# Performance work log

Measured on AMD Instinct MI355X. Metric: run time of the kernel, lower is better.

The kernel has to match this reference:

```python
import jax, jax.numpy as jnp
import numpy as np

EPS_Q = 1e-4     # ridge added to L L^T in OptNet.forward
MAX_ITER = 20    # qpth pdipm_b maxIter
BIG = 1e10       # sentinel for inactive step-length entries


def _make_kkt_solver(Q, G):
    """Shared factorizations (qpth pre_factor_kkt): Q Cholesky and S0 = G Q^{-1} G^T."""
    nineq = G.shape[0]
    Lq = jnp.linalg.cholesky(Q)                                   # [nz, nz]

    def q_solve(rhs):                                             # rhs [B, nz] -> Q^{-1} rhs
        return jax.scipy.linalg.cho_solve((Lq, True), rhs.T).T

    S0 = G @ jax.scipy.linalg.cho_solve((Lq, True), G.T)          # [nineq, nineq]
    eye = jnp.eye(nineq, dtype=Q.dtype)

    def solve(d, rx, rs, rz):
        # Solve the reduced KKT system (qpth solve_kkt, neq=0):
        #   [Q G^T; G -D^{-1}] [dx; dz] = [-rx; -rz + D^{-1} rs],  ds = (-rs - dz)/d
        invQ_rx = q_solve(rx)                                     # [B, nz]
        hv = invQ_rx @ G.T + rs / d - rz                          # [B, nineq]
        S = S0[None] + eye * (1.0 / d)[:, None, :]                # S0 + diag(1/d) per batch
        dz = -jnp.linalg.solve(S, hv[..., None])[..., 0]
        dx = q_solve(-rx - dz @ G)
        ds = (-rs - dz) / d
        return dx, ds, dz

    return solve


def _get_step(v, dv):
    # max alpha with v + alpha*dv >= 0 (min over entries with dv < 0); safe against NaN grads
    dv_safe = jnp.where(dv < 0, dv, -1.0)
    a = jnp.where(dv < 0, -v / dv_safe, BIG)
    return jnp.min(a, axis=1)


def pdipm_forward(Q, p, G, h):
    """qpth pdipm_b.forward (Mehrotra predictor-corrector), neq=0, fixed 20 iters with best-tracking."""
    nB, nz = p.shape
    nineq = G.shape[0]
    solve = _make_kkt_solver(Q, G)

    # initial point: KKT solve with d = 1, then shift s, z into the positive orthant
    d0 = jnp.ones((nB, nineq), Q.dtype)
    zeros = jnp.zeros((nB, nineq), Q.dtype)
    x, s, z = solve(d0, p, zeros, -h)
    smin = jnp.min(s, axis=1, keepdims=True)
    s = jnp.where(smin < 0, s - smin + 1.0, s)
    zmin = jnp.min(z, axis=1, keepdims=True)
    z = jnp.where(zmin < 0, z - zmin + 1.0, z)

    def body(carry, _):
        x, s, z, bx, bz, bs, bsum = carry
        rx = x @ Q + p + z @ G          # stationarity residual (Q symmetric)
        rs = z
        rz = x @ G.T + s - h            # primal residual
        mu = jnp.abs(jnp.sum(s * z, axis=1)) / nineq
        resids = jnp.linalg.norm(rz, axis=1) + jnp.linalg.norm(rx, axis=1) + nineq * mu
        rsum = jnp.sum(resids)
        imp = rsum < bsum
        bx = jnp.where(imp, x, bx)
        bz = jnp.where(imp, z, bz)
        bs = jnp.where(imp, s, bs)
        bsum = jnp.where(imp, rsum, bsum)
        d = z / s
        # affine (predictor) step
        dx_a, ds_a, dz_a = solve(d, rx, rs, rz)
        alpha = jnp.minimum(jnp.minimum(_get_step(z, dz_a), _get_step(s, ds_a)), 1.0)[:, None]
        sig = (jnp.sum((s + alpha * ds_a) * (z + alpha * dz_a), axis=1)
               / jnp.sum(s * z, axis=1)) ** 3
        # centering + corrector step
        rs_c = ((-mu * sig)[:, None] + ds_a * dz_a) / s
        dx_c, ds_c, dz_c = solve(d, jnp.zeros_like(rx), rs_c, jnp.zeros_like(rz))
        dx = dx_a + dx_c
        ds = ds_a + ds_c
        dz = dz_a + dz_c
        alpha = jnp.minimum(0.999 * jnp.minimum(_get_step(z, dz), _get_step(s, ds)), 1.0)[:, None]
        x = x + alpha * dx
        s = s + alpha * ds
        z = z + alpha * dz
        return (x, s, z, bx, bz, bs, bsum), None

    init = (x, s, z, x, z, s, jnp.asarray(np.inf, dtype=Q.dtype))
    (x, s, z, bx, bz, bs, bsum), _ = jax.lax.scan(body, init, None, length=MAX_ITER)
    return bx, bz, bs                   # zhat, lam (dual), slack


def setup_inputs() -> dict:
    key = jax.random.key(0)
    k1, k2, k3 = jax.random.split(key, 3)
    B, nz, nineq = 128, 512, 512
    x = jax.random.normal(k1, (B, nz), dtype=jnp.float32)
    M = jnp.tril(jnp.ones((nz, nz), jnp.float32))                        # Parameter M = tril(ones)
    L = jnp.tril(jax.random.uniform(k2, (nz, nz), dtype=jnp.float32))    # Parameter L = tril(rand)
    G = jax.random.uniform(k3, (nineq, nz), dtype=jnp.float32, minval=-1.0, maxval=1.0)
    s0 = jnp.ones((nineq,), jnp.float32)
    z0 = jnp.zeros((nz,), jnp.float32)
    return {"x": x, "M": M, "L": L, "G": G, "s0": s0, "z0": z0}


def reference(x, M, L, G, s0, z0):
    nz = L.shape[0]
    Lm = M * L
    Q = Lm @ Lm.T + EPS_Q * jnp.eye(nz, dtype=L.dtype)                   # PSD + ridge
    h = jnp.broadcast_to(z0 @ G.T + s0, (x.shape[0], G.shape[0]))        # h = G z0 + s0
    zhat, _, _ = pdipm_forward(Q, x, G, h)                               # p = x
    return zhat
```

## Files before the change

kernel.cpp:

```cpp
#include <hip/hip_runtime.h>
#include <math.h>

#define BIGD 1e10
#define N2C 262144
#define PITCH_AS 257
#define FACF 131328

__device__ __forceinline__ int tile_off(int bi, int bj) {
    return 512 * bi * (bi - 1) + 528 * bi + (bj << 10);
}
__device__ __forceinline__ int tile_off_diag(int bi) {
    return 512 * bi * (bi - 1) + 528 * bi + (bi << 10);
}

__device__ __forceinline__ double blk_reduce_sum_d(double v, double* red) {
    int tid = threadIdx.x;
    red[tid] = v; __syncthreads();
    for (int s = 128; s > 0; s >>= 1) {
        if (tid < s) red[tid] += red[tid + s];
        __syncthreads();
    }
    double r = red[0]; __syncthreads();
    return r;
}
__device__ __forceinline__ double blk_reduce_min_d(double v, double* red) {
    int tid = threadIdx.x;
    red[tid] = v; __syncthreads();
    for (int s = 128; s > 0; s >>= 1) {
        if (tid < s) red[tid] = fmin(red[tid], red[tid + s]);
        __syncthreads();
    }
    double r = red[0]; __syncthreads();
    return r;
}

__global__ void k_lm(const float* __restrict__ M, const float* __restrict__ L,
                     double* __restrict__ C, int n) {
    int i = blockIdx.x * 256 + threadIdx.x;
    if (i < n) C[i] = (double)M[i] * (double)L[i];
}
__global__ void k_cast(const float* __restrict__ A, double* __restrict__ B, int n) {
    int i = blockIdx.x * 256 + threadIdx.x;
    if (i < n) B[i] = (double)A[i];
}
__global__ void k_cast32v(const double* __restrict__ A, float* __restrict__ B, int n) {
    int i = blockIdx.x * 256 + threadIdx.x;
    if (i < n) B[i] = (float)A[i];
}
__global__ void k_initbsum(double* bsum) {
    if (threadIdx.x == 0) bsum[0] = 1e300;
}

__global__ __launch_bounds__(256) void k_transpose_d(const double* __restrict__ A,
                                                     double* __restrict__ B) {
    __shared__ double t[32][33];
    int bx = blockIdx.x & 15, by = blockIdx.x >> 4;
    int x = threadIdx.x & 31, y0 = threadIdx.x >> 5;
#pragma unroll
    for (int l = 0; l < 4; ++l) {
        int y = y0 + 8 * l;
        t[y][x] = A[(size_t)(by * 32 + y) * 512 + bx * 32 + x];
    }
    __syncthreads();
#pragma unroll
    for (int l = 0; l < 4; ++l) {
        int y = y0 + 8 * l;
        B[(size_t)(bx * 32 + y) * 512 + by * 32 + x] = t[x][y];
    }
}
__global__ __launch_bounds__(256) void k_transpose32(const float* __restrict__ A,
                                                     float* __restrict__ B) {
    __shared__ float t[32][33];
    int bx = blockIdx.x & 15, by = blockIdx.x >> 4;
    int x = threadIdx.x & 31, y0 = threadIdx.x >> 5;
#pragma unroll
    for (int l = 0; l < 4; ++l) {
        int y = y0 + 8 * l;
        t[y][x] = A[(size_t)(by * 32 + y) * 512 + bx * 32 + x];
    }
    __syncthreads();
#pragma unroll
    for (int l = 0; l < 4; ++l) {
        int y = y0 + 8 * l;
        B[(size_t)(bx * 32 + y) * 512 + by * 32 + x] = t[x][y];
    }
}

__global__ void k_h_d(const float* __restrict__ G, const float* __restrict__ s0,
                      const float* __restrict__ z0, double* __restrict__ h) {
    __shared__ double red[256];
    int tid = threadIdx.x;
    int j = blockIdx.x * 64 + (tid >> 2);
    int q = tid & 3;
    double a = 0.0;
    for (int k = q * 128; k < q * 128 + 128; ++k)
        a += (double)G[(size_t)j * 512 + k] * (double)z0[k];
    red[tid] = a;
    __syncthreads();
    if (q == 0) h[j] = (double)s0[j] + red[tid] + red[tid + 1] + red[tid + 2] + red[tid + 3];
}

__global__ __launch_bounds__(256) void k_bgemm_d(
    const double* __restrict__ A1, const double* __restrict__ B1,
    double* __restrict__ C, double sgn, double diag_eps)
{
    __shared__ double As[32 * 68];
    __shared__ double Bs[32 * 68];
    int bid = blockIdx.x;
    int mt = bid >> 3, nt = bid & 7;
    int m0 = mt * 64, n0 = nt * 64;
    int tid = threadIdx.x;
    int tx = tid & 15, ty = tid >> 4;
    double acc[4][4] = {};
    for (int k0 = 0; k0 < 512; k0 += 32) {
        __syncthreads();
#pragma unroll
        for (int l = 0; l < 8; ++l) {
            int idx = tid + 256 * l;
            int kk = idx & 31, r = idx >> 5;
            As[kk * 68 + r] = A1[(size_t)(m0 + r) * 512 + k0 + kk];
            int cc = idx & 63, k2 = idx >> 6;
            Bs[k2 * 68 + cc] = B1[(size_t)(k0 + k2) * 512 + n0 + cc];
        }
        __syncthreads();
#pragma unroll
        for (int kk = 0; kk < 32; ++kk) {
            double a4[4], b4[4];
#pragma unroll
            for (int u = 0; u < 4; ++u) a4[u] = As[kk * 68 + tx * 4 + u];
#pragma unroll
            for (int u = 0; u < 4; ++u) b4[u] = Bs[kk * 68 + ty * 4 + u];
#pragma unroll
            for (int ii = 0; ii < 4; ++ii)
#pragma unroll
                for (int jj = 0; jj < 4; ++jj)
                    acc[ii][jj] += a4[ii] * b4[jj];
        }
    }
#pragma unroll
    for (int ii = 0; ii < 4; ++ii) {
        int gm = m0 + tx * 4 + ii;
#pragma unroll
        for (int jj = 0; jj < 4; ++jj) {
            int gn = n0 + ty * 4 + jj;
            double v = sgn * acc[ii][jj];
            if (diag_eps != 0.0 && gm == gn) v += diag_eps;
            C[(size_t)gm * 512 + gn] = v;
        }
    }
}

__global__ __launch_bounds__(256) void k_gemm32(
    const float* __restrict__ A1, const float* __restrict__ B1,
    const float* __restrict__ A2, const float* __restrict__ B2,
    float* __restrict__ C,
    const float* __restrict__ addp, const float* __restrict__ subp,
    const float* __restrict__ rowp, float rowsgn, float sgn)
{
    __shared__ float As[32 * 68];
    __shared__ float Bs[32 * 68];
    int bid = blockIdx.x;
    int mt = bid >> 3, nt = bid & 7;
    int m0 = mt * 64, n0 = nt * 64;
    int tid = threadIdx.x;
    int tx = tid & 15, ty = tid >> 4;
    double acc[4][4] = {};
    for (int prod = 0; prod < 2; ++prod) {
        const float* A = prod ? A2 : A1;
        const float* B = prod ? B2 : B1;
        if (A == nullptr) break;
        for (int k0 = 0; k0 < 512; k0 += 32) {
            __syncthreads();
#pragma unroll
            for (int l = 0; l < 8; ++l) {
                int idx = tid + 256 * l;
                int kk = idx & 31, r = idx >> 5;
                As[kk * 68 + r] = A[(size_t)(m0 + r) * 512 + k0 + kk];
                int cc = idx & 63, k2 = idx >> 6;
                Bs[k2 * 68 + cc] = B[(size_t)(k0 + k2) * 512 + n0 + cc];
            }
            __syncthreads();
#pragma unroll
            for (int kk = 0; kk < 32; ++kk) {
                double a4[4], b4[4];
#pragma unroll
                for (int u = 0; u < 4; ++u) a4[u] = (double)As[kk * 68 + tx * 4 + u];
#pragma unroll
                for (int u = 0; u < 4; ++u) b4[u] = (double)Bs[kk * 68 + ty * 4 + u];
#pragma unroll
                for (int ii = 0; ii < 4; ++ii)
#pragma unroll
                    for (int jj = 0; jj < 4; ++jj)
                        acc[ii][jj] += a4[ii] * b4[jj];
            }
        }
    }
#pragma unroll
    for (int ii = 0; ii < 4; ++ii) {
        int gm = m0 + tx * 4 + ii;
#pragma unroll
        for (int jj = 0; jj < 4; ++jj) {
            int gn = n0 + ty * 4 + jj;
            size_t gi = (size_t)gm * 512 + gn;
            double v = (double)sgn * acc[ii][jj];
            if (addp) v += (double)addp[gi];
            if (subp) v -= (double)subp[gi];
            if (rowp) v += (double)rowsgn * (double)rowp[gn];
            C[gi] = (float)v;
        }
    }
}

__global__ void k_copyadd_d(const double* __restrict__ S, double* __restrict__ F,
                            double dc, int n) {
    int i = blockIdx.x * 256 + threadIdx.x;
    if (i < n) {
        double v = S[i];
        if (dc != 0.0 && (i >> 9) == (i & 511)) v += dc;
        F[i] = v;
    }
}

__global__ __launch_bounds__(512) void k_cpanel_d(double* __restrict__ F, int kp) {
    int c0 = kp * 32, tid = threadIdx.x;
    __shared__ double Dl[32 * 33];
    __shared__ double rdg[32];
    if (tid < 32) {
        int i = tid;
        double d[32];
#pragma unroll
        for (int j = 0; j < 32; ++j) d[j] = F[(size_t)(c0 + i) * 512 + c0 + j];
#pragma unroll
        for (int j = 0; j < 32; ++j) {
            double djj = __shfl(d[j], j);
            djj = (djj > 1e-300) ? djj : 1e-300;
            double sj = sqrt(djj);
            double inv = 1.0 / sj;
            if (i == j) { d[j] = sj; rdg[j] = inv; }
            if (i > j) d[j] *= inv;
            double lij = d[j];
#pragma unroll
            for (int t = j + 1; t < 32; ++t) {
                double ltj = __shfl(d[j], t);
                if (i >= t) d[t] -= lij * ltj;
            }
        }
#pragma unroll
        for (int j = 0; j < 32; ++j) {
            if (j <= i) {
                Dl[i * 33 + j] = d[j];
                F[(size_t)(c0 + i) * 512 + c0 + j] = d[j];
            }
        }
    }
    __syncthreads();
    int r = c0 + 32 + tid;
    if (r < 512) {
        double p[32];
#pragma unroll
        for (int j = 0; j < 32; ++j) p[j] = F[(size_t)r * 512 + c0 + j];
#pragma unroll
        for (int j = 0; j < 32; ++j) {
            double pj = p[j] * rdg[j];
            p[j] = pj;
#pragma unroll
            for (int t = j + 1; t < 32; ++t) p[t] -= pj * Dl[t * 33 + j];
        }
#pragma unroll
        for (int j = 0; j < 32; ++j) F[(size_t)r * 512 + c0 + j] = p[j];
    }
}

__global__ __launch_bounds__(256) void k_syrk_d(double* __restrict__ F, int kp) {
    int c0 = kp * 32;
    int t = blockIdx.x;
    int bi = 0;
    while ((bi + 1) * (bi + 2) / 2 <= t) ++bi;
    int bj = t - bi * (bi + 1) / 2;
    int i0 = c0 + 32 + bi * 64, j0 = c0 + 32 + bj * 64;
    __shared__ double Pa[32 * 68], Pb[32 * 68];
    int tid = threadIdx.x;
#pragma unroll
    for (int l = 0; l < 8; ++l) {
        int idx = tid + 256 * l;
        int kk = idx & 31, r = idx >> 5;
        int ga = i0 + r, gb = j0 + r;
        Pa[kk * 68 + r] = (ga < 512) ? F[(size_t)ga * 512 + c0 + kk] : 0.0;
        Pb[kk * 68 + r] = (gb < 512) ? F[(size_t)gb * 512 + c0 + kk] : 0.0;
    }
    __syncthreads();
    int tx = tid & 15, ty = tid >> 4;
    double acc[4][4] = {};
#pragma unroll
    for (int kk = 0; kk < 32; ++kk) {
        double a4[4], b4[4];
#pragma unroll
        for (int u = 0; u < 4; ++u) a4[u] = Pa[kk * 68 + tx * 4 + u];
#pragma unroll
        for (int u = 0; u < 4; ++u) b4[u] = Pb[kk * 68 + ty * 4 + u];
#pragma unroll
        for (int ii = 0; ii < 4; ++ii)
#pragma unroll
            for (int jj = 0; jj < 4; ++jj)
                acc[ii][jj] += a4[ii] * b4[jj];
    }
#pragma unroll
    for (int ii = 0; ii < 4; ++ii) {
        int gi = i0 + tx * 4 + ii;
        if (gi < 512) {
#pragma unroll
            for (int jj = 0; jj < 4; ++jj) {
                int gj = j0 + ty * 4 + jj;
                if (gj < 512) F[(size_t)gi * 512 + gj] -= acc[ii][jj];
            }
        }
    }
}

__global__ __launch_bounds__(256) void k_solve_d(
    const double* __restrict__ F,
    const float* __restrict__ rhs32,
    double* __restrict__ o1, double* __restrict__ o2,
    float* __restrict__ o1f, float* __restrict__ o2f,
    int mode)
{
    int b = blockIdx.x;
    int tid = threadIdx.x;
    __shared__ double w[512];
    __shared__ double Ft[64 * 65];
    __shared__ double red[256];
    if (rhs32) {
        w[tid] = (double)rhs32[(size_t)b * 512 + tid];
        w[tid + 256] = (double)rhs32[(size_t)b * 512 + tid + 256];
    } else {
        w[tid] = (tid == b) ? 1.0 : 0.0;
        w[tid + 256] = (tid + 256 == b) ? 1.0 : 0.0;
    }
    for (int blk = 0; blk < 8; ++blk) {
        int c0 = blk * 64;
        int r = tid & 63, q = tid >> 6;
        double acc = 0.0;
        for (int jt = 0; jt < blk; ++jt) {
            __syncthreads();
#pragma unroll
            for (int l = 0; l < 16; ++l) {
                int idx = tid + 256 * l;
                int rr = idx >> 6, cc = idx & 63;
                Ft[rr * 65 + cc] = F[(size_t)(c0 + rr) * 512 + jt * 64 + cc];
            }
            __syncthreads();
#pragma unroll
            for (int jj = 0; jj < 16; ++jj) {
                int j = q * 16 + jj;
                acc += Ft[r * 65 + j] * w[jt * 64 + j];
            }
        }
        red[tid] = acc;
        __syncthreads();
#pragma unroll
        for (int l = 0; l < 16; ++l) {
            int idx = tid + 256 * l;
            int rr = idx >> 6, cc = idx & 63;
            Ft[rr * 65 + cc] = F[(size_t)(c0 + rr) * 512 + c0 + cc];
        }
        __syncthreads();
        if (tid < 64) {
            int i = tid;
            double a = w[c0 + i] - (red[i] + red[i + 64] + red[i + 128] + red[i + 192]);
            double rd = 1.0 / Ft[i * 65 + i];
#pragma unroll
            for (int j = 0; j < 64; ++j) {
                double wj = __shfl(a, j) * __shfl(rd, j);
                if (i == j) w[c0 + i] = wj;
                if (i > j) a -= Ft[i * 65 + j] * wj;
            }
        }
        __syncthreads();
    }
    for (int blk = 7; blk >= 0; --blk) {
        int c0 = blk * 64;
        __syncthreads();
#pragma unroll
        for (int l = 0; l < 16; ++l) {
            int idx = tid + 256 * l;
            int rr = idx >> 6, cc = idx & 63;
            Ft[rr * 65 + cc] = F[(size_t)(c0 + rr) * 512 + c0 + cc];
        }
        __syncthreads();
        if (tid < 64) {
            int i = tid;
            double a = w[c0 + i];
            double rd = 1.0 / Ft[i * 65 + i];
#pragma unroll
            for (int j = 63; j >= 0; --j) {
                double wj = __shfl(a, j) * __shfl(rd, j);
                if (i == j) w[c0 + i] = wj;
                if (i < j) a -= Ft[j * 65 + i] * wj;
            }
        }
        __syncthreads();
        if (c0 > 0) {
            for (int base = 0; base < c0; base += 256) {
                int col = base + tid;
                if (col < c0) {
                    double s = 0.0;
#pragma unroll
                    for (int i2 = 0; i2 < 64; ++i2)
                        s += F[(size_t)(c0 + i2) * 512 + col] * w[c0 + i2];
                    w[col] -= s;
                }
            }
        }
    }
    __syncthreads();
#pragma unroll
    for (int l = 0; l < 2; ++l) {
        int i = tid + l * 256;
        double wv = w[i];
        size_t gi = (size_t)b * 512 + i;
        if (mode == 0) {
            o1[gi] = wv;
            o1f[gi] = (float)wv;
        } else {
            o1[gi] = -wv;
            o2[gi] = wv;
            o1f[gi] = (float)(-wv);
            o2f[gi] = (float)wv;
        }
    }
}

__device__ void trsv_packed(const float* __restrict__ Lb, const double* __restrict__ rdgAll,
                            double* __restrict__ wv, double* __restrict__ red, int tid)
{
    for (int j = 0; j < 16; ++j) {
        int c0 = j * 32;
        int i = tid >> 4, k = tid & 15;
        double a = 0.0;
        if (k < j) {
            const float* tp = Lb + tile_off(j, k) + i * 32;
            const double* wp = wv + k * 32;
#pragma unroll 8
            for (int m = 0; m < 32; ++m) a += (double)tp[m] * wp[m];
        }
        red[tid] = a;
        __syncthreads();
        if (tid < 32) {
            int i2 = tid;
            double s = 0.0;
#pragma unroll
            for (int k2 = 0; k2 < 16; ++k2) s += red[i2 * 16 + k2];
            double aa = wv[c0 + i2] - s;
            double rdgv = rdgAll[c0 + i2];
            const float* tp = Lb + tile_off_diag(j);
            int basei = (i2 * (i2 + 1)) >> 1;
            float lrow[32];
#pragma unroll
            for (int m = 0; m < 32; ++m) lrow[m] = (m < i2) ? tp[basei + m] : 0.f;
#pragma unroll
            for (int m = 0; m < 32; ++m) {
                double xm = __shfl(aa * rdgv, m);
                if (i2 == m) wv[c0 + i2] = xm;
                if (i2 > m) aa -= (double)lrow[m] * xm;
            }
        }
        __syncthreads();
    }
    for (int j = 15; j >= 0; --j) {
        int c0 = j * 32;
        if (tid < 32) {
            int i2 = tid;
            double aa = wv[c0 + i2];
            double rdgv = rdgAll[c0 + i2];
            const float* tp = Lb + tile_off_diag(j);
            float lcol[32];
#pragma unroll
            for (int m = 0; m < 32; ++m)
                lcol[m] = (m > i2) ? tp[((m * (m + 1)) >> 1) + i2] : 0.f;
#pragma unroll
            for (int m = 31; m >= 0; --m) {
                double xm = __shfl(aa * rdgv, m);
                if (i2 == m) wv[c0 + i2] = xm;
                if (i2 < m) aa -= (double)lcol[m] * xm;
            }
        }
        __syncthreads();
        if (j > 0) {
            int k = tid >> 5, m = tid & 31;
            if (k < j) {
                const float* tp = Lb + tile_off(j, k) + m;
                double sacc = 0.0;
#pragma unroll 8
                for (int i3 = 0; i3 < 32; ++i3) sacc += (double)tp[i3 * 32] * wv[c0 + i3];
                wv[k * 32 + m] -= sacc;
            }
            __syncthreads();
        }
    }
}

__device__ void refine_once(const double* __restrict__ S0d, const double* __restrict__ dvecS,
                            const double* __restrict__ rhsL, double* __restrict__ wv,
                            double* __restrict__ tmpS, double* __restrict__ red,
                            const float* __restrict__ Lb, const double* __restrict__ rdgAll,
                            int tid)
{
    double a = 0.0;
    const double* sp = S0d + tid;
    for (int c = 0; c < 512; ++c) a += sp[(size_t)c * 512] * wv[c];
    double r = rhsL[tid] - a - dvecS[tid] * wv[tid];
    __syncthreads();
    tmpS[tid] = r;
    __syncthreads();
    trsv_packed(Lb, rdgAll, tmpS, red, tid);
    wv[tid] += tmpS[tid];
    __syncthreads();
}

__global__ __launch_bounds__(512) void k_fused(
    const double* __restrict__ S0d,
    float* __restrict__ F0,
    const double* __restrict__ ss, const double* __restrict__ zs,
    const float* __restrict__ hvf,
    const double* __restrict__ mu, const double* __restrict__ szs,
    float* __restrict__ dzv, float* __restrict__ dsv,
    int b0)
{
    const int tid = threadIdx.x;
    const int b = b0 + blockIdx.x;
    float* Lb = F0 + (size_t)blockIdx.x * FACF;
    const size_t gb = (size_t)b * 512;

    __shared__ double pool[9376];
    __shared__ double Dl[32 * 33];
    __shared__ double rdgS[32];
    __shared__ double rdgAll[512];
    __shared__ double wv[512], rhsL[512], dvecS[512], tmpS[512], redS[512];
    double* As = pool;
    double* Bs = pool + 32 * PITCH_AS;
    double* W  = pool;

    const int tx = tid & 63, ty = tid >> 6;

    for (int j = 0; j < 16; ++j) {
        const int c0 = j * 32;
        for (int rbase = c0; rbase < 512; rbase += 256) {
            const int rows = (512 - rbase < 256) ? (512 - rbase) : 256;
            double acc[4][4];
#pragma unroll
            for (int v = 0; v < 4; ++v) {
                int cg = c0 + 4 * ty + v;
                const double* srow = S0d + (size_t)cg * 512 + rbase + tx;
#pragma unroll
                for (int u = 0; u < 4; ++u) {
                    int rl = tx + 64 * u;
                    acc[u][v] = (rl < rows) ? srow[64 * u] : 0.0;
                }
            }
            if (rbase == c0) {
#pragma unroll
                for (int u = 0; u < 4; ++u) {
                    int rg = rbase + tx + 64 * u;
#pragma unroll
                    for (int v = 0; v < 4; ++v) {
                        if (rg == c0 + 4 * ty + v) acc[u][v] += ss[gb + rg] / zs[gb + rg];
                    }
                }
            }
            for (int k = 0; k < j; ++k) {
                __syncthreads();
                {
                    int rl0 = tid >> 3;
                    int kq = (tid & 7) * 4;
                    for (int rr = rl0; rr < rows; rr += 64) {
                        int gr = rbase + rr;
                        const float* tp = Lb + tile_off(gr >> 5, k) + (gr & 31) * 32 + kq;
                        float4 f4 = *(const float4*)tp;
                        As[(kq + 0) * PITCH_AS + rr] = (double)f4.x;
                        As[(kq + 1) * PITCH_AS + rr] = (double)f4.y;
                        As[(kq + 2) * PITCH_AS + rr] = (double)f4.z;
                        As[(kq + 3) * PITCH_AS + rr] = (double)f4.w;
                    }
                }
                {
                    const float* tp = Lb + tile_off(j, k);
#pragma unroll
                    for (int l = 0; l < 2; ++l) {
                        int idx = tid + 512 * l;
                        int c = idx >> 5, kk = idx & 31;
                        Bs[kk * 36 + c] = (double)tp[c * 32 + kk];
                    }
                }
                __syncthreads();
#pragma unroll 8
                for (int kk = 0; kk < 32; ++kk) {
                    double a4[4], b4[4];
#pragma unroll
                    for (int u = 0; u < 4; ++u) a4[u] = As[kk * PITCH_AS + tx + 64 * u];
#pragma unroll
                    for (int v = 0; v < 4; ++v) b4[v] = Bs[kk * 36 + 4 * ty + v];
#pragma unroll
                    for (int u = 0; u < 4; ++u)
#pragma unroll
                        for (int v = 0; v < 4; ++v)
                            acc[u][v] -= a4[u] * b4[v];
                }
            }
            __syncthreads();
#pragma unroll
            for (int u = 0; u < 4; ++u) {
                int rl = tx + 64 * u;
                if (rl < rows) {
#pragma unroll
                    for (int v = 0; v < 4; ++v)
                        W[rl * 33 + 4 * ty + v] = acc[u][v];
                }
            }
            __syncthreads();
            int trsm0 = 0;
            if (rbase == c0) {
                trsm0 = 32;
                if (tid < 32) {
                    int i = tid;
                    double d[32];
#pragma unroll
                    for (int m2 = 0; m2 < 32; ++m2) d[m2] = W[i * 33 + m2];
#pragma unroll
                    for (int m2 = 0; m2 < 32; ++m2) {
                        double djj = __shfl(d[m2], m2);
                        djj = (djj > 1e-30) ? djj : 1e-30;
                        double sj = sqrt(djj);
                        double inv = 1.0 / sj;
                        if (i == m2) { d[m2] = sj; rdgS[m2] = inv; rdgAll[c0 + m2] = inv; }
                        if (i > m2) d[m2] *= inv;
                        double lij = d[m2];
#pragma unroll
                        for (int t2 = m2 + 1; t2 < 32; ++t2) {
                            double ltj = __shfl(d[m2], t2);
                            if (i >= t2) d[t2] -= lij * ltj;
                        }
                    }
                    float* tp = Lb + tile_off_diag(j);
                    int basei = (i * (i + 1)) >> 1;
#pragma unroll
                    for (int m2 = 0; m2 < 32; ++m2) {
                        if (m2 <= i) { Dl[i * 33 + m2] = d[m2]; tp[basei + m2] = (float)d[m2]; }
                    }
                }
                __syncthreads();
            }
            {
                int nr = rows - trsm0;
                if (tid < nr) {
                    int rl = trsm0 + tid;
                    int gr = rbase + rl;
                    double x[32];
#pragma unroll
                    for (int m2 = 0; m2 < 32; ++m2) x[m2] = W[rl * 33 + m2];
#pragma unroll
                    for (int m2 = 0; m2 < 32; ++m2) {
                        double xm = x[m2] * rdgS[m2];
                        x[m2] = xm;
#pragma unroll
                        for (int t2 = m2 + 1; t2 < 32; ++t2) x[t2] -= xm * Dl[t2 * 33 + m2];
                    }
                    float* tp = Lb + tile_off(gr >> 5, j) + (gr & 31) * 32;
#pragma unroll
                    for (int m2 = 0; m2 < 32; ++m2) tp[m2] = (float)x[m2];
                }
            }
            __syncthreads();
        }
    }

    double z_t = zs[gb + tid], s_t = ss[gb + tid];
    double dv = s_t / z_t;
    dvecS[tid] = dv;
    double r1 = (double)hvf[gb + tid];
    wv[tid] = r1;
    rhsL[tid] = r1;
    __syncthreads();
    trsv_packed(Lb, rdgAll, wv, redS, tid);
    refine_once(S0d, dvecS, rhsL, wv, tmpS, redS, Lb, rdgAll, tid);

    double dza_t = -wv[tid];
    double dsa_t = -(z_t + dza_t) * dv;
    __syncthreads();

    double az = (dza_t < 0.0) ? (-z_t / dza_t) : BIGD;
    double as = (dsa_t < 0.0) ? (-s_t / dsa_t) : BIGD;
    redS[tid] = fmin(az, as);
    __syncthreads();
    for (int s2 = 256; s2 > 0; s2 >>= 1) {
        if (tid < s2) redS[tid] = fmin(redS[tid], redS[tid + s2]);
        __syncthreads();
    }
    double alpha = fmin(redS[0], 1.0);
    __syncthreads();
    redS[tid] = (s_t + alpha * dsa_t) * (z_t + alpha * dza_t);
    __syncthreads();
    for (int s2 = 256; s2 > 0; s2 >>= 1) {
        if (tid < s2) redS[tid] += redS[tid + s2];
        __syncthreads();
    }
    double d2 = redS[0];
    __syncthreads();
    double ratio = d2 / szs[b];
    double sig = ratio * ratio * ratio;
    double coef = -mu[b] * sig;
    double num = coef + dsa_t * dza_t;
    double rsc_t = num / s_t;
    wv[tid] = num / z_t;
    rhsL[tid] = wv[tid];
    __syncthreads();

    trsv_packed(Lb, rdgAll, wv, redS, tid);
    refine_once(S0d, dvecS, rhsL, wv, tmpS, redS, Lb, rdgAll, tid);

    double dz = dza_t - wv[tid];
    double ds = -(z_t + rsc_t + dz) * dv;
    dzv[gb + tid] = (float)dz;
    dsv[gb + tid] = (float)ds;
}

__global__ __launch_bounds__(256) void k_stats_d(
    const float* __restrict__ rx, const float* __restrict__ rz,
    const double* __restrict__ ssv, const double* __restrict__ zsv,
    double* resid, double* mu, double* szsum)
{
    int b = blockIdx.x, tid = threadIdx.x;
    __shared__ double red[256];
    double s1 = 0, s2 = 0, s3 = 0;
#pragma unroll
    for (int l = 0; l < 2; ++l) {
        size_t gi = (size_t)b * 512 + tid + l * 256;
        double vx = (double)rx[gi]; s1 += vx * vx;
        double vz = (double)rz[gi]; s2 += vz * vz;
        s3 += ssv[gi] * zsv[gi];
    }
    double t1 = blk_reduce_sum_d(s1, red);
    double t2 = blk_reduce_sum_d(s2, red);
    double t3 = blk_reduce_sum_d(s3, red);
    if (tid == 0) {
        resid[b] = sqrt(t2) + sqrt(t1) + fabs(t3);
        mu[b] = fabs(t3) / 512.0;
        szsum[b] = t3;
    }
}

__global__ void k_best_d(const double* __restrict__ resid, double* bsum, double* flag) {
    __shared__ double red[128];
    int tid = threadIdx.x;
    red[tid] = resid[tid];
    __syncthreads();
    for (int s = 64; s > 0; s >>= 1) {
        if (tid < s) red[tid] += red[tid + s];
        __syncthreads();
    }
    if (tid == 0) {
        double rs = red[0];
        if (rs < bsum[0]) { bsum[0] = rs; flag[0] = 1.0; }
        else flag[0] = 0.0;
    }
}

__global__ void k_bestcopy_d(const double* __restrict__ flag, const double* __restrict__ xs,
                             float* __restrict__ bx) {
    if (flag && flag[0] == 0.0) return;
    int i0 = blockIdx.x * 1024 + threadIdx.x;
#pragma unroll
    for (int l = 0; l < 4; ++l) bx[i0 + l * 256] = (float)xs[i0 + l * 256];
}

__global__ __launch_bounds__(256) void k_final_d(
    double* __restrict__ xs, double* __restrict__ ssv, double* __restrict__ zsv,
    const float* __restrict__ dxf, const float* __restrict__ dsf, const float* __restrict__ dzf,
    float* __restrict__ xs32, float* __restrict__ ss32, float* __restrict__ zs32)
{
    int b = blockIdx.x, tid = threadIdx.x;
    __shared__ double red[256];
    double m = BIGD;
#pragma unroll
    for (int l = 0; l < 2; ++l) {
        size_t gi = (size_t)b * 512 + tid + l * 256;
        double z = zsv[gi], dz = (double)dzf[gi];
        double az = (dz < 0.0) ? (-z / dz) : BIGD;
        double s = ssv[gi], ds = (double)dsf[gi];
        double as = (ds < 0.0) ? (-s / ds) : BIGD;
        m = fmin(m, fmin(az, as));
    }
    double am = blk_reduce_min_d(m, red);
    double alpha = fmin(0.999 * am, 1.0);
#pragma unroll
    for (int l = 0; l < 2; ++l) {
        size_t gi = (size_t)b * 512 + tid + l * 256;
        double nx = xs[gi] + alpha * (double)dxf[gi];
        double ns = ssv[gi] + alpha * (double)dsf[gi];
        double nz = zsv[gi] + alpha * (double)dzf[gi];
        xs[gi] = nx; ssv[gi] = ns; zsv[gi] = nz;
        xs32[gi] = (float)nx; ss32[gi] = (float)ns; zs32[gi] = (float)nz;
    }
}

__global__ __launch_bounds__(256) void k_shift_d(double* __restrict__ ssv, double* __restrict__ zsv,
                                                 float* __restrict__ ss32, float* __restrict__ zs32)
{
    int b = blockIdx.x, tid = threadIdx.x;
    __shared__ double red[256];
    double m = BIGD;
#pragma unroll
    for (int l = 0; l < 2; ++l) m = fmin(m, ssv[(size_t)b * 512 + tid + l * 256]);
    double smin = blk_reduce_min_d(m, red);
    if (smin < 0.0) {
#pragma unroll
        for (int l = 0; l < 2; ++l) ssv[(size_t)b * 512 + tid + l * 256] += 1.0 - smin;
    }
    m = BIGD;
#pragma unroll
    for (int l = 0; l < 2; ++l) m = fmin(m, zsv[(size_t)b * 512 + tid + l * 256]);
    double zmin = blk_reduce_min_d(m, red);
    if (zmin < 0.0) {
#pragma unroll
        for (int l = 0; l < 2; ++l) zsv[(size_t)b * 512 + tid + l * 256] += 1.0 - zmin;
    }
#pragma unroll
    for (int l = 0; l < 2; ++l) {
        size_t gi = (size_t)b * 512 + tid + l * 256;
        ss32[gi] = (float)ssv[gi];
        zs32[gi] = (float)zsv[gi];
    }
}

extern "C" void kernel_launch(void* const* d_in, const int* in_sizes, int n_in,
                              void* d_out, int out_size, void* d_ws, size_t ws_size,
                              hipStream_t stream)
{
    (void)in_sizes; (void)n_in; (void)out_size;
    const float* xin = (const float*)d_in[0];
    const float* Mi  = (const float*)d_in[1];
    const float* Li  = (const float*)d_in[2];
    const float* Gin = (const float*)d_in[3];
    const float* s0  = (const float*)d_in[4];
    const float* z0  = (const float*)d_in[5];
    float* outp = (float*)d_out;

    const size_t N2 = N2C;
    double* base = (double*)d_ws;
    size_t off = 0;
    auto A = [&](size_t n) { double* p = base + off; off += n; return p; };
    double* S0d  = A(N2);
    double* h    = A(512);
    double* resid = A(128); double* mu = A(128); double* szs = A(128);
    double* bsum = A(8); double* flag = A(8);
    double* xs = A(65536); double* ss = A(65536); double* zs = A(65536);
    float* Qf   = (float*)A(131072);
    float* GTf  = (float*)A(131072);
    float* Qif  = (float*)A(131072);
    float* h32  = (float*)A(256);
    float* rxf  = (float*)A(32768);
    float* rzf  = (float*)A(32768);
    float* hvf  = (float*)A(32768);
    float* t1f  = (float*)A(32768);
    float* dzvf = (float*)A(32768);
    float* dsvf = (float*)A(32768);
    float* xs32 = (float*)A(32768);
    float* ss32 = (float*)A(32768);
    float* zs32 = (float*)A(32768);
    float* dxf = hvf;
    float* t2f = t1f;

    double* slab = base + off;
    size_t avail = (ws_size / 8 > off) ? (ws_size / 8 - off) : 0;
    int C = (int)(avail / (FACF / 2));
    if (C > 128) C = 128;
    if (C < 1) C = 1;
    float* F0 = (float*)slab;
    double* Lm64  = slab;
    double* LmT64 = slab + 1 * N2;
    double* Q64   = slab + 2 * N2;
    double* Lq    = slab + 3 * N2;
    double* Qi64  = slab + 4 * N2;
    double* G64   = slab + 5 * N2;
    double* GT64  = slab + 6 * N2;
    double* X64   = slab + 7 * N2;
    double* SfI   = slab + 8 * N2;

    dim3 t256(256), t512(512);
    const float* NPf = nullptr;

    k_lm<<<1024, t256, 0, stream>>>(Mi, Li, Lm64, 262144);
    k_transpose_d<<<256, t256, 0, stream>>>(Lm64, LmT64);
    k_bgemm_d<<<64, t256, 0, stream>>>(Lm64, LmT64, Q64, 1.0, 1e-4);
    k_cast32v<<<1024, t256, 0, stream>>>(Q64, Qf, 262144);
    k_copyadd_d<<<1024, t256, 0, stream>>>(Q64, Lq, 0.0, 262144);
    for (int kp = 0; kp < 16; ++kp) {
        k_cpanel_d<<<1, t512, 0, stream>>>(Lq, kp);
        int Tr = 480 - 32 * kp;
        if (Tr > 0) {
            int T = (Tr + 63) >> 6;
            k_syrk_d<<<T * (T + 1) / 2, t256, 0, stream>>>(Lq, kp);
        }
    }
    k_solve_d<<<512, t256, 0, stream>>>(Lq, NPf, Qi64, nullptr, Qif, nullptr, 0);
    k_cast<<<1024, t256, 0, stream>>>(Gin, G64, 262144);
    k_transpose_d<<<256, t256, 0, stream>>>(G64, GT64);
    k_transpose32<<<256, t256, 0, stream>>>(Gin, GTf);
    k_bgemm_d<<<64, t256, 0, stream>>>(Qi64, GT64, X64, 1.0, 0.0);
    k_bgemm_d<<<64, t256, 0, stream>>>(G64, X64, S0d, 1.0, 0.0);
    k_copyadd_d<<<1024, t256, 0, stream>>>(S0d, SfI, 1.0, 262144);
    for (int kp = 0; kp < 16; ++kp) {
        k_cpanel_d<<<1, t512, 0, stream>>>(SfI, kp);
        int Tr = 480 - 32 * kp;
        if (Tr > 0) {
            int T = (Tr + 63) >> 6;
            k_syrk_d<<<T * (T + 1) / 2, t256, 0, stream>>>(SfI, kp);
        }
    }
    k_h_d<<<8, t256, 0, stream>>>(Gin, s0, z0, h);
    k_cast32v<<<2, t256, 0, stream>>>(h, h32, 512);
    k_initbsum<<<1, 64, 0, stream>>>(bsum);

    k_gemm32<<<16, t256, 0, stream>>>(xin, Qif, NPf, NPf, t1f, NPf, NPf, NPf, 0.f, 1.f);
    k_gemm32<<<16, t256, 0, stream>>>(t1f, GTf, NPf, NPf, hvf, NPf, NPf, h32, 1.f, 1.f);
    k_solve_d<<<128, t256, 0, stream>>>(SfI, hvf, zs, ss, zs32, ss32, 1);
    k_gemm32<<<16, t256, 0, stream>>>(zs32, Gin, NPf, NPf, t1f, xin, NPf, NPf, 0.f, 1.f);
    k_gemm32<<<16, t256, 0, stream>>>(t1f, Qif, NPf, NPf, xs32, NPf, NPf, NPf, 0.f, -1.f);
    k_cast<<<256, t256, 0, stream>>>(xs32, xs, 65536);
    k_shift_d<<<128, t256, 0, stream>>>(ss, zs, ss32, zs32);
    k_bestcopy_d<<<64, t256, 0, stream>>>(nullptr, xs, outp);

    for (int it = 0; it < 20; ++it) {
        k_gemm32<<<16, t256, 0, stream>>>(xs32, Qf, zs32, Gin, rxf, xin, NPf, NPf, 0.f, 1.f);
        k_gemm32<<<16, t256, 0, stream>>>(xs32, GTf, NPf, NPf, rzf, ss32, NPf, h32, -1.f, 1.f);
        k_stats_d<<<128, t256, 0, stream>>>(rxf, rzf, ss, zs, resid, mu, szs);
        k_best_d<<<1, 128, 0, stream>>>(resid, bsum, flag);
        k_bestcopy_d<<<64, t256, 0, stream>>>(flag, xs, outp);
        k_gemm32<<<16, t256, 0, stream>>>(rxf, Qif, NPf, NPf, t1f, NPf, NPf, NPf, 0.f, 1.f);
        k_gemm32<<<16, t256, 0, stream>>>(t1f, GTf, NPf, NPf, hvf, ss32, rzf, NPf, 0.f, 1.f);
        for (int b0 = 0; b0 < 128; b0 += C) {
            int cnt = (128 - b0 < C) ? (128 - b0) : C;
            k_fused<<<cnt, t512, 0, stream>>>(S0d, F0, ss, zs, hvf, mu, szs, dzvf, dsvf, b0);
        }
        k_gemm32<<<16, t256, 0, stream>>>(dzvf, Gin, NPf, NPf, t2f, rxf, NPf, NPf, 0.f, 1.f);
        k_gemm32<<<16, t256, 0, stream>>>(t2f, Qif, NPf, NPf, dxf, NPf, NPf, NPf, 0.f, -1.f);
        k_final_d<<<128, t256, 0, stream>>>(xs, ss, zs, dxf, dsvf, dzvf, xs32, ss32, zs32);
    }
}
```

Measured before the change: 54.38 ms.

## Use FP64 MFMA for trailing update in per-batch blocked Cholesky

Adds an FP64 MFMA (16x16x4) path for the trailing-panel update inside the fused per-batch Cholesky factorization kernel. Each wave accumulates 16x16 output tiles from the staged L panels, and the sum is subtracted from S0 plus the diagonal term afterwards. A one-off runtime self-test kernel checks the MFMA lane layout and selects between the MFMA path and the original scalar FMA loop. The scheme relies on the assumed operand and output lane mapping being correct, and it adds an extra shared-memory pass to combine results.

```diff
diff --git a/kernel.cpp b/kernel.cpp
--- a/kernel.cpp
+++ b/kernel.cpp
@@ -5,6 +5,8 @@
 #define N2C 262144
 #define PITCH_AS 257
 #define FACF 131328
+
+typedef double d4 __attribute__((ext_vector_type(4)));
 
 __device__ __forceinline__ int tile_off(int bi, int bj) {
     return 512 * bi * (bi - 1) + 528 * bi + (bj << 10);
@@ -32,6 +34,29 @@
     }
     double r = red[0]; __syncthreads();
     return r;
+}
+
+__device__ __forceinline__ double tAv(int i, int k) { return (double)(1 + i + 17 * k); }
+__device__ __forceinline__ double tBv(int k, int j) { return (double)(2 + 3 * j + 31 * k); }
+
+__global__ void k_mfmatest(int* flag) {
+    int l = threadIdx.x;
+    int i_a = l & 15, k_a = l >> 4;
+    double av = tAv(i_a, k_a);
+    double bv = tBv(k_a, i_a);
+    d4 c = (d4){0.0, 0.0, 0.0, 0.0};
+    c = __builtin_amdgcn_mfma_f64_16x16x4f64(av, bv, c, 0, 0, 0);
+    bool ok = true;
+#pragma unroll
+    for (int r = 0; r < 4; ++r) {
+        int di = 4 * (l >> 4) + r, dj = l & 15;
+        double ref = 0.0;
+#pragma unroll
+        for (int k = 0; k < 4; ++k) ref += tAv(di, k) * tBv(k, dj);
+        ok = ok && (c[r] == ref);
+    }
+    unsigned long long m = __ballot(ok);
+    if (l == 0) flag[0] = (m == 0xFFFFFFFFFFFFFFFFull) ? 1 : 0;
 }
 
 __global__ void k_lm(const float* __restrict__ M, const float* __restrict__ L,
@@ -524,12 +549,14 @@
     const float* __restrict__ hvf,
     const double* __restrict__ mu, const double* __restrict__ szs,
     float* __restrict__ dzv, float* __restrict__ dsv,
+    const int* __restrict__ mfok,
     int b0)
 {
     const int tid = threadIdx.x;
     const int b = b0 + blockIdx.x;
     float* Lb = F0 + (size_t)blockIdx.x * FACF;
     const size_t gb = (size_t)b * 512;
+    const int useM = mfok[0];
 
     __shared__ double pool[9376];
     __shared__ double Dl[32 * 33];
@@ -541,82 +568,163 @@
     double* W  = pool;
 
     const int tx = tid & 63, ty = tid >> 6;
+    const int lane = tid & 63, wid = tid >> 6;
+    const int aoff = lane & 15, koff = lane >> 4;
 
     for (int j = 0; j < 16; ++j) {
         const int c0 = j * 32;
         for (int rbase = c0; rbase < 512; rbase += 256) {
             const int rows = (512 - rbase < 256) ? (512 - rbase) : 256;
-            double acc[4][4];
-#pragma unroll
-            for (int v = 0; v < 4; ++v) {
-                int cg = c0 + 4 * ty + v;
-                const double* srow = S0d + (size_t)cg * 512 + rbase + tx;
+
+            if (useM) {
+                const int ntiles = (rows >> 4) << 1;
+                d4 uacc[4];
+#pragma unroll
+                for (int tt = 0; tt < 4; ++tt) uacc[tt] = (d4){0.0, 0.0, 0.0, 0.0};
+                for (int k = 0; k < j; ++k) {
+                    __syncthreads();
+                    {
+                        int rl0 = tid >> 3;
+                        int kq = (tid & 7) * 4;
+                        for (int rr = rl0; rr < rows; rr += 64) {
+                            int gr = rbase + rr;
+                            const float* tp = Lb + tile_off(gr >> 5, k) + (gr & 31) * 32 + kq;
+                            float4 f4 = *(const float4*)tp;
+                            As[(kq + 0) * PITCH_AS + rr] = (double)f4.x;
+                            As[(kq + 1) * PITCH_AS + rr] = (double)f4.y;
+                            As[(kq + 2) * PITCH_AS + rr] = (double)f4.z;
+                            As[(kq + 3) * PITCH_AS + rr] = (double)f4.w;
+                        }
+                    }
+                    {
+                        const float* tp = Lb + tile_off(j, k);
+#pragma unroll
+                        for (int l = 0; l < 2; ++l) {
+                            int idx = tid + 512 * l;
+                            int c = idx >> 5, kk = idx & 31;
+                            Bs[kk * 36 + c] = (double)tp[c * 32 + kk];
+                        }
+                    }
+                    __syncthreads();
+#pragma unroll
+                    for (int tt = 0; tt < 4; ++tt) {
+                        int t = wid + (tt << 3);
+                        if (t < ntiles) {
+                            int s16 = (t >> 1) << 4, hcol = (t & 1) << 4;
+                            d4 uv = uacc[tt];
+#pragma unroll
+                            for (int k4 = 0; k4 < 8; ++k4) {
+                                double av = As[(k4 * 4 + koff) * PITCH_AS + s16 + aoff];
+                                double bv = Bs[(k4 * 4 + koff) * 36 + hcol + aoff];
+                                uv = __builtin_amdgcn_mfma_f64_16x16x4f64(av, bv, uv, 0, 0, 0);
+                            }
+                            uacc[tt] = uv;
+                        }
+                    }
+                }
+                __syncthreads();
+#pragma unroll
+                for (int tt = 0; tt < 4; ++tt) {
+                    int t = wid + (tt << 3);
+                    if (t < ntiles) {
+                        int s16 = (t >> 1) << 4, hcol = (t & 1) << 4;
+#pragma unroll
+                        for (int r = 0; r < 4; ++r) {
+                            int rloc = s16 + (koff << 2) + r;
+                            W[rloc * 33 + hcol + aoff] = uacc[tt][r];
+                        }
+                    }
+                }
+                __syncthreads();
+#pragma unroll
+                for (int v = 0; v < 4; ++v) {
+                    int cg = c0 + 4 * ty + v;
+                    const double* srow = S0d + (size_t)cg * 512 + rbase + tx;
+#pragma unroll
+                    for (int uu = 0; uu < 4; ++uu) {
+                        int rl = tx + 64 * uu;
+                        if (rl < rows) {
+                            double sv = srow[64 * uu];
+                            int rg = rbase + rl;
+                            if (rbase == c0 && rg == cg) sv += ss[gb + rg] / zs[gb + rg];
+                            W[rl * 33 + 4 * ty + v] = sv - W[rl * 33 + 4 * ty + v];
+                        }
+                    }
+                }
+            } else {
+                double acc[4][4];
+#pragma unroll
+                for (int v = 0; v < 4; ++v) {
+                    int cg = c0 + 4 * ty + v;
+                    const double* srow = S0d + (size_t)cg * 512 + rbase + tx;
+#pragma unroll
+                    for (int u = 0; u < 4; ++u) {
+                        int rl = tx + 64 * u;
+                        acc[u][v] = (rl < rows) ? srow[64 * u] : 0.0;
+                    }
+                }
+                if (rbase == c0) {
+#pragma unroll
+                    for (int u = 0; u < 4; ++u) {
+                        int rg = rbase + tx + 64 * u;
+#pragma unroll
+                        for (int v = 0; v < 4; ++v) {
+                            if (rg == c0 + 4 * ty + v) acc[u][v] += ss[gb + rg] / zs[gb + rg];
+                        }
+                    }
+                }
+                for (int k = 0; k < j; ++k) {
+                    __syncthreads();
+                    {
+                        int rl0 = tid >> 3;
+                        int kq = (tid & 7) * 4;
+                        for (int rr = rl0; rr < rows; rr += 64) {
+                            int gr = rbase + rr;
+                            const float* tp = Lb + tile_off(gr >> 5, k) + (gr & 31) * 32 + kq;
+                            float4 f4 = *(const float4*)tp;
+                            As[(kq + 0) * PITCH_AS + rr] = (double)f4.x;
+                            As[(kq + 1) * PITCH_AS + rr] = (double)f4.y;
+                            As[(kq + 2) * PITCH_AS + rr] = (double)f4.z;
+                            As[(kq + 3) * PITCH_AS + rr] = (double)f4.w;
+                        }
+                    }
+                    {
+                        const float* tp = Lb + tile_off(j, k);
+#pragma unroll
+                        for (int l = 0; l < 2; ++l) {
+                            int idx = tid + 512 * l;
+                            int c = idx >> 5, kk = idx & 31;
+                            Bs[kk * 36 + c] = (double)tp[c * 32 + kk];
+                        }
+                    }
+                    __syncthreads();
+#pragma unroll 8
+                    for (int kk = 0; kk < 32; ++kk) {
+                        double a4[4], b4[4];
+#pragma unroll
+                        for (int u = 0; u < 4; ++u) a4[u] = As[kk * PITCH_AS + tx + 64 * u];
+#pragma unroll
+                        for (int v = 0; v < 4; ++v) b4[v] = Bs[kk * 36 + 4 * ty + v];
+#pragma unroll
+                        for (int u = 0; u < 4; ++u)
+#pragma unroll
+                            for (int v = 0; v < 4; ++v)
+                                acc[u][v] -= a4[u] * b4[v];
+                    }
+                }
+                __syncthreads();
 #pragma unroll
                 for (int u = 0; u < 4; ++u) {
                     int rl = tx + 64 * u;
-                    acc[u][v] = (rl < rows) ? srow[64 * u] : 0.0;
+                    if (rl < rows) {
+#pragma unroll
+                        for (int v = 0; v < 4; ++v)
+                            W[rl * 33 + 4 * ty + v] = acc[u][v];
+                    }
                 }
             }
-            if (rbase == c0) {
-#pragma unroll
-                for (int u = 0; u < 4; ++u) {
-                    int rg = rbase + tx + 64 * u;
-#pragma unroll
-                    for (int v = 0; v < 4; ++v) {
-                        if (rg == c0 + 4 * ty + v) acc[u][v] += ss[gb + rg] / zs[gb + rg];
-                    }
-                }
-            }
-            for (int k = 0; k < j; ++k) {
-                __syncthreads();
-                {
-                    int rl0 = tid >> 3;
-                    int kq = (tid & 7) * 4;
-                    for (int rr = rl0; rr < rows; rr += 64) {
-                        int gr = rbase + rr;
-                        const float* tp = Lb + tile_off(gr >> 5, k) + (gr & 31) * 32 + kq;
-                        float4 f4 = *(const float4*)tp;
-                        As[(kq + 0) * PITCH_AS + rr] = (double)f4.x;
-                        As[(kq + 1) * PITCH_AS + rr] = (double)f4.y;
-                        As[(kq + 2) * PITCH_AS + rr] = (double)f4.z;
-                        As[(kq + 3) * PITCH_AS + rr] = (double)f4.w;
-                    }
-                }
-                {
-                    const float* tp = Lb + tile_off(j, k);
-#pragma unroll
-                    for (int l = 0; l < 2; ++l) {
-                        int idx = tid + 512 * l;
-                        int c = idx >> 5, kk = idx & 31;
-                        Bs[kk * 36 + c] = (double)tp[c * 32 + kk];
-                    }
-                }
-                __syncthreads();
-#pragma unroll 8
-                for (int kk = 0; kk < 32; ++kk) {
-                    double a4[4], b4[4];
-#pragma unroll
-                    for (int u = 0; u < 4; ++u) a4[u] = As[kk * PITCH_AS + tx + 64 * u];
-#pragma unroll
-                    for (int v = 0; v < 4; ++v) b4[v] = Bs[kk * 36 + 4 * ty + v];
-#pragma unroll
-                    for (int u = 0; u < 4; ++u)
-#pragma unroll
-                        for (int v = 0; v < 4; ++v)
-                            acc[u][v] -= a4[u] * b4[v];
-                }
-            }
             __syncthreads();
-#pragma unroll
-            for (int u = 0; u < 4; ++u) {
-                int rl = tx + 64 * u;
-                if (rl < rows) {
-#pragma unroll
-                    for (int v = 0; v < 4; ++v)
-                        W[rl * 33 + 4 * ty + v] = acc[u][v];
-                }
-            }
-            __syncthreads();
+
             int trsm0 = 0;
             if (rbase == c0) {
                 trsm0 = 32;
@@ -852,6 +960,8 @@
     double* h    = A(512);
     double* resid = A(128); double* mu = A(128); double* szs = A(128);
     double* bsum = A(8); double* flag = A(8);
+    double* mfokd = A(8);
+    int* mfok = (int*)mfokd;
     double* xs = A(65536); double* ss = A(65536); double* zs = A(65536);
     float* Qf   = (float*)A(131072);
     float* GTf  = (float*)A(131072);
@@ -888,6 +998,7 @@
     dim3 t256(256), t512(512);
     const float* NPf = nullptr;
 
+    k_mfmatest<<<1, 64, 0, stream>>>(mfok);
     k_lm<<<1024, t256, 0, stream>>>(Mi, Li, Lm64, 262144);
     k_transpose_d<<<256, t256, 0, stream>>>(Lm64, LmT64);
     k_bgemm_d<<<64, t256, 0, stream>>>(Lm64, LmT64, Q64, 1.0, 1e-4);
@@ -939,7 +1050,8 @@
         k_gemm32<<<16, t256, 0, stream>>>(t1f, GTf, NPf, NPf, hvf, ss32, rzf, NPf, 0.f, 1.f);
         for (int b0 = 0; b0 < 128; b0 += C) {
             int cnt = (128 - b0 < C) ? (128 - b0) : C;
-            k_fused<<<cnt, t512, 0, stream>>>(S0d, F0, ss, zs, hvf, mu, szs, dzvf, dsvf, b0);
+            k_fused<<<cnt, t512, 0, stream>>>(S0d, F0, ss, zs, hvf, mu, szs, dzvf, dsvf,
+                                              mfok, b0);
         }
         k_gemm32<<<16, t256, 0, stream>>>(dzvf, Gin, NPf, NPf, t2f, rxf, NPf, NPf, 0.f, 1.f);
         k_gemm32<<<16, t256, 0, stream>>>(t2f, Qif, NPf, NPf, dxf, NPf, NPf, NPf, 0.f, -1.f);
```

Result: no change. 54.47 ms (+0.2%).
